# Kernel tuning notes

Hardware: AMD Instinct MI355X
Metric: run time of the kernel (lower is better)

Reference implementation:

```python
import jax, jax.numpy as jnp
import numpy as np
from math import sqrt

D_MODEL = 1024
NUM_HEADS = 16
MASK_VAL = -100000000.0


def setup_inputs() -> dict:
    key = jax.random.key(0)
    k1, k2, k3, k4, k5 = jax.random.split(key, 5)
    scale = 1.0 / sqrt(D_MODEL)
    return {
        "in_features": jax.random.normal(k1, (2, 2048, D_MODEL), dtype=jnp.float32),
        "q_proj_weight": jax.random.normal(k2, (D_MODEL, D_MODEL), dtype=jnp.float32) * scale,
        "k_proj_weight": jax.random.normal(k3, (D_MODEL, D_MODEL), dtype=jnp.float32) * scale,
        "v_proj_weight": jax.random.normal(k4, (D_MODEL, D_MODEL), dtype=jnp.float32) * scale,
        "o_proj_weight": jax.random.normal(k5, (D_MODEL, D_MODEL), dtype=jnp.float32) * scale,
    }


def _proj_heads(x, w, h):
    # x: [b, s, d_in], w: [h*d, d_in] -> [b, h, s, d]
    d = w.shape[0] // h
    w = w.reshape(h, d, w.shape[1])
    return jnp.einsum('bsi,hdi->bhsd', x, w)


def reference(in_features, q_proj_weight, k_proj_weight, v_proj_weight, o_proj_weight):
    h = NUM_HEADS
    b, s, _ = in_features.shape
    q = _proj_heads(in_features, q_proj_weight, h)  # [b,h,s,dk]
    k = _proj_heads(in_features, k_proj_weight, h)
    v = _proj_heads(in_features, v_proj_weight, h)
    d_k = q.shape[-1]
    # additive causal mask: -1e8 above diagonal
    mask = jnp.triu(jnp.full((s, s), MASK_VAL, dtype=q.dtype), k=1)[None, None]
    scores = jnp.einsum('bhqd,bhkd->bhqk', q, k) / sqrt(d_k) + mask
    attn = jax.nn.softmax(scores, axis=-1)
    out = jnp.einsum('bhqk,bhkd->bhqd', attn, v)          # [b,h,s,dv]
    out = out.transpose(0, 2, 1, 3).reshape(b, s, -1)      # [b,s,h*dv]
    return jnp.einsum('bsv,mv->bsm', out, o_proj_weight)
```

## Files before the change

kernel.cpp:

```cpp
#include <hip/hip_runtime.h>
#include <hip/hip_bf16.h>
#include <stdint.h>
#include <type_traits>

typedef __bf16 bf16;
typedef __bf16 bf16x4 __attribute__((ext_vector_type(4)));
typedef __bf16 bf16x8 __attribute__((ext_vector_type(8)));
typedef float floatx4 __attribute__((ext_vector_type(4)));
typedef unsigned int u32;

#define D_MODEL 1024
#define SEQ 2048
#define NHEADS 16
#define DH 64
#define BATCH 2
#define MROWS (BATCH * SEQ)

#define XELEMS ((size_t)MROWS * D_MODEL)
#define WELEMS ((size_t)D_MODEL * D_MODEL)
#define CVT_ELEMS (XELEMS + 4 * WELEMS)

__device__ __forceinline__ void gload_lds16(const void* g, void* l) {
  __builtin_amdgcn_global_load_lds(
      (const __attribute__((address_space(1))) u32*)g,
      (__attribute__((address_space(3))) u32*)l, 16, 0, 0);
}

__global__ __launch_bounds__(256) void cvt_f32_bf16(
    const float* __restrict__ s0, const float* __restrict__ s1,
    const float* __restrict__ s2, const float* __restrict__ s3,
    const float* __restrict__ s4, bf16* __restrict__ dst) {
  const size_t i = ((size_t)blockIdx.x * 256 + threadIdx.x) * 8;
  const float* src;
  size_t off;
  if (i < XELEMS) {
    src = s0; off = i;
  } else {
    const size_t j = i - XELEMS;
    const int r = (int)(j / WELEMS);
    src = (r == 0) ? s1 : (r == 1) ? s2 : (r == 2) ? s3 : s4;
    off = j - (size_t)r * WELEMS;
  }
  floatx4 f0 = *(const floatx4*)&src[off];
  floatx4 f1 = *(const floatx4*)&src[off + 4];
  bf16x8 o;
#pragma unroll
  for (int j = 0; j < 4; j++) { o[j] = (bf16)f0[j]; o[4 + j] = (bf16)f1[j]; }
  *(bf16x8*)&dst[i] = o;
}

#define QKV_ASLOT (256 * 64)
#define QKV_SLOT  (256 * 64 + 128 * 64)

__global__ __launch_bounds__(512) void gemm_qkv(
    const bf16* __restrict__ A, const bf16* __restrict__ W,
    bf16* __restrict__ Qo, bf16* __restrict__ Ko, bf16* __restrict__ Vto) {
  __shared__ bf16 sm[3 * QKV_SLOT];

  const int tid = threadIdx.x;
  const int lane = tid & 63;
  const int w = tid >> 6;
  const int lo16 = lane & 15;
  const int quad = lane >> 4;
  const int wy = w >> 1;
  const int wx = w & 1;

  const int n0 = blockIdx.x * 128;
  const int m0 = blockIdx.y * 256;

  const int sl = lane >> 3;
  const int sc = ((lane & 7) ^ sl) * 8;

  const floatx4 fz = {0.f, 0.f, 0.f, 0.f};
  floatx4 acc[4][4];
#pragma unroll
  for (int i = 0; i < 4; i++)
#pragma unroll
    for (int j = 0; j < 4; j++) acc[i][j] = fz;

  auto stage = [&](int t, int s) {
    bf16* As = &sm[s * QKV_SLOT];
    bf16* Bs = As + QKV_ASLOT;
    const int k0 = t * 64;
#pragma unroll
    for (int i = 0; i < 4; i++) {
      const int seg = w * 4 + i;
      const int row = seg * 8 + sl;
      gload_lds16(&A[(size_t)(m0 + row) * 1024 + k0 + sc], &As[seg * 512]);
    }
#pragma unroll
    for (int i = 0; i < 2; i++) {
      const int seg = w * 2 + i;
      const int row = seg * 8 + sl;
      gload_lds16(&W[(size_t)(n0 + row) * 1024 + k0 + sc], &Bs[seg * 512]);
    }
  };

  auto compute = [&](int s, auto vt) {
    constexpr bool VT = decltype(vt)::value;
    const bf16* As = &sm[s * QKV_SLOT];
    const bf16* Bs = As + QKV_ASLOT;
#pragma unroll
    for (int kk = 0; kk < 64; kk += 32) {
      bf16x8 af[4], bfr[4];
      const int cc = (kk >> 3) + quad;
#pragma unroll
      for (int t = 0; t < 4; t++) {
        const int ra = wy * 64 + t * 16 + lo16;
        const int rb = wx * 64 + t * 16 + lo16;
        af[t]  = *(const bf16x8*)&As[ra * 64 + ((cc ^ (ra & 7)) << 3)];
        bfr[t] = *(const bf16x8*)&Bs[rb * 64 + ((cc ^ (rb & 7)) << 3)];
      }
#pragma unroll
      for (int mt = 0; mt < 4; mt++)
#pragma unroll
        for (int nt = 0; nt < 4; nt++) {
          if constexpr (VT)
            acc[mt][nt] = __builtin_amdgcn_mfma_f32_16x16x32_bf16(bfr[nt], af[mt], acc[mt][nt], 0, 0, 0);
          else
            acc[mt][nt] = __builtin_amdgcn_mfma_f32_16x16x32_bf16(af[mt], bfr[nt], acc[mt][nt], 0, 0, 0);
        }
    }
  };

  auto step = [&](int t, int s, auto vt) {
    if (t + 2 < 16) stage(t + 2, (t + 2) % 3);
    compute(s, vt);
    if (t < 15) {
      if (t + 2 < 16) { asm volatile("s_waitcnt vmcnt(6)" ::: "memory"); }
      else            { asm volatile("s_waitcnt vmcnt(0)" ::: "memory"); }
      __builtin_amdgcn_s_barrier();
    }
  };

  auto mainloop = [&](auto vt) {
    stage(0, 0);
    stage(1, 1);
    asm volatile("s_waitcnt vmcnt(6)" ::: "memory");
    __builtin_amdgcn_s_barrier();
    for (int tb = 0; tb < 15; tb += 3) {
      step(tb + 0, 0, vt);
      step(tb + 1, 1, vt);
      step(tb + 2, 2, vt);
    }
    step(15, 0, vt);
  };
  if (n0 >= 2048) mainloop(std::true_type{}); else mainloop(std::false_type{});

  if (n0 < 2048) {
    bf16* C = (n0 < 1024) ? Qo : Ko;
    const int nc = (n0 < 1024) ? n0 : n0 - 1024;
#pragma unroll
    for (int mt = 0; mt < 4; mt++)
#pragma unroll
      for (int nt = 0; nt < 4; nt++)
#pragma unroll
        for (int r = 0; r < 4; r++) {
          const int row = m0 + wy * 64 + mt * 16 + quad * 4 + r;
          const int col = nc + wx * 64 + nt * 16 + lo16;
          C[(size_t)row * D_MODEL + col] = (bf16)acc[mt][nt][r];
        }
  } else {
    const int nv = n0 - 2048;
#pragma unroll
    for (int mt = 0; mt < 4; mt++)
#pragma unroll
      for (int nt = 0; nt < 4; nt++)
#pragma unroll
        for (int r = 0; r < 4; r++) {
          const int feat = nv + wx * 64 + nt * 16 + quad * 4 + r;
          const int tok  = m0 + wy * 64 + mt * 16 + lo16;
          const int hh = feat >> 6, dd = feat & 63;
          const int bb = tok >> 11, ss = tok & 2047;
          Vto[(size_t)((bb * NHEADS + hh) * DH + dd) * SEQ + ss] = (bf16)acc[mt][nt][r];
        }
  }
}

__global__ __launch_bounds__(256) void gemm_o(
    const bf16* __restrict__ A, const bf16* __restrict__ W,
    float* __restrict__ C) {
  __shared__ bf16 As[2 * 64 * 64];
  __shared__ bf16 Bs[2 * 128 * 64];

  const int tid = threadIdx.x;
  const int lane = tid & 63;
  const int w = tid >> 6;
  const int lo16 = lane & 15;
  const int quad = lane >> 4;
  const int wy = w >> 1, wx = w & 1;

  const int m0 = blockIdx.y * 64;
  const int n0 = blockIdx.x * 128;

  const int sl = lane >> 3;
  const int sc = ((lane & 7) ^ sl) * 8;

  const floatx4 fz = {0.f, 0.f, 0.f, 0.f};
  floatx4 acc[2][4];
#pragma unroll
  for (int i = 0; i < 2; i++)
#pragma unroll
    for (int j = 0; j < 4; j++) acc[i][j] = fz;

  for (int k0 = 0; k0 < 1024; k0 += 128) {
    __syncthreads();
#pragma unroll
    for (int kh = 0; kh < 2; kh++) {
#pragma unroll
      for (int i = 0; i < 2; i++) {
        const int seg = i * 4 + w;
        const int row = seg * 8 + sl;
        gload_lds16(&A[(size_t)(m0 + row) * 1024 + k0 + kh * 64 + sc],
                    &As[kh * 4096 + seg * 512]);
      }
#pragma unroll
      for (int i = 0; i < 4; i++) {
        const int seg = i * 4 + w;
        const int row = seg * 8 + sl;
        gload_lds16(&W[(size_t)(n0 + row) * 1024 + k0 + kh * 64 + sc],
                    &Bs[kh * 8192 + seg * 512]);
      }
    }
    __syncthreads();

#pragma unroll
    for (int kk = 0; kk < 128; kk += 32) {
      const int kh = kk >> 6;
      const int cc = ((kk & 63) >> 3) + quad;
      bf16x8 af[2], bfr[4];
#pragma unroll
      for (int t = 0; t < 2; t++) {
        const int ra = wy * 32 + t * 16 + lo16;
        af[t] = *(const bf16x8*)&As[kh * 4096 + ra * 64 + ((cc ^ (ra & 7)) << 3)];
      }
#pragma unroll
      for (int t = 0; t < 4; t++) {
        const int rb = wx * 64 + t * 16 + lo16;
        bfr[t] = *(const bf16x8*)&Bs[kh * 8192 + rb * 64 + ((cc ^ (rb & 7)) << 3)];
      }
#pragma unroll
      for (int mt = 0; mt < 2; mt++)
#pragma unroll
        for (int nt = 0; nt < 4; nt++)
          acc[mt][nt] = __builtin_amdgcn_mfma_f32_16x16x32_bf16(af[mt], bfr[nt], acc[mt][nt], 0, 0, 0);
    }
  }

#pragma unroll
  for (int mt = 0; mt < 2; mt++)
#pragma unroll
    for (int nt = 0; nt < 4; nt++)
#pragma unroll
      for (int r = 0; r < 4; r++) {
        const int row = m0 + wy * 32 + mt * 16 + quad * 4 + r;
        const int col = n0 + wx * 64 + nt * 16 + lo16;
        C[(size_t)row * D_MODEL + col] = acc[mt][nt][r];
      }
}

#define LPK 72
#define LPV 136
#define LPP 72

__global__ __launch_bounds__(512, 4) void attn_causal(
    const bf16* __restrict__ Q, const bf16* __restrict__ Kg,
    const bf16* __restrict__ Vt, bf16* __restrict__ O) {
  __shared__ __align__(16) char smem[54272];
  bf16* Ks  = (bf16*)smem;
  bf16* VTs = (bf16*)(smem + 18432);
  bf16* Ps  = (bf16*)(smem + 35840);
  float* Es = (float*)smem;

  const int tid = threadIdx.x;
  const int lane = tid & 63;
  const int wid = tid >> 6;
  const int g = wid >> 2;
  const int w4 = wid & 3;
  const int lo16 = lane & 15;
  const int quad = lane >> 4;

  const int x = blockIdx.x;
  const int qtA = x;
  const int qtB = 31 - x;
  const int nA = (qtA + 2) >> 1;
  const int nB = (qtB + 2) >> 1;
  const int h = blockIdx.y;
  const int b = blockIdx.z;
  const size_t base  = (size_t)b * SEQ * D_MODEL + (size_t)h * DH;
  const size_t baset = (size_t)(b * NHEADS + h) * DH * SEQ;

  const int rA = qtA * 64 + w4 * 16 + lo16;
  const int rB = qtB * 64 + w4 * 16 + lo16;
  bf16x8 qfA[2], qfB[2];
#pragma unroll
  for (int ks = 0; ks < 2; ks++) {
    qfA[ks] = *(const bf16x8*)&Q[base + (size_t)rA * D_MODEL + ks * 32 + quad * 8];
    qfB[ks] = *(const bf16x8*)&Q[base + (size_t)rB * D_MODEL + ks * 32 + quad * 8];
  }

  bf16x8 onesf;
#pragma unroll
  for (int j = 0; j < 8; j++) onesf[j] = (bf16)1.0f;

  const floatx4 fz = {0.f, 0.f, 0.f, 0.f};
  floatx4 oA[4], oB[4];
  floatx4 lA = fz, lB = fz;
#pragma unroll
  for (int i = 0; i < 4; i++) { oA[i] = fz; oB[i] = fz; }

  const int kr = tid >> 3;
  const int kc = (tid & 7) * 8;

  bf16x8 kvp[2], vvp[2];
#pragma unroll
  for (int c2 = 0; c2 < 2; c2++) {
    kvp[c2] = *(const bf16x8*)&Kg[base + (size_t)(c2 * 64 + kr) * D_MODEL + kc];
    vvp[c2] = *(const bf16x8*)&Vt[baset + (size_t)kr * SEQ + c2 * 64 + kc];
  }

  for (int c = 0; c < nB; c++) {
    const int j0 = c * 128;
    __syncthreads();
#pragma unroll
    for (int c2 = 0; c2 < 2; c2++) {
      *(bf16x8*)&Ks[(c2 * 64 + kr) * LPK + kc] = kvp[c2];
      *(bf16x8*)&VTs[kr * LPV + c2 * 64 + kc] = vvp[c2];
    }
    __syncthreads();

    if (c + 1 < nB) {
      const int j1 = j0 + 128;
#pragma unroll
      for (int c2 = 0; c2 < 2; c2++) {
        kvp[c2] = *(const bf16x8*)&Kg[base + (size_t)(j1 + c2 * 64 + kr) * D_MODEL + kc];
        vvp[c2] = *(const bf16x8*)&Vt[baset + (size_t)kr * SEQ + j1 + c2 * 64 + kc];
      }
    }

    auto compute = [&](int q0s, const bf16x8* qf, floatx4* oacc, floatx4& lacc,
                       bool diag) {
      floatx4 sacc[4];
#pragma unroll
      for (int n = 0; n < 4; n++) sacc[n] = fz;
#pragma unroll
      for (int n = 0; n < 4; n++) {
        const int rk = g * 64 + n * 16 + lo16;
#pragma unroll
        for (int ks = 0; ks < 2; ks++) {
          bf16x8 kf = *(const bf16x8*)&Ks[rk * LPK + ks * 32 + quad * 8];
          sacc[n] = __builtin_amdgcn_mfma_f32_16x16x32_bf16(kf, qf[ks], sacc[n], 0, 0, 0);
        }
      }

      if (diag) {
        const int myq = q0s + w4 * 16 + lo16;
#pragma unroll
        for (int n = 0; n < 4; n++) {
          const int kvb = j0 + g * 64 + n * 16 + quad * 4;
          bf16x4 pk;
#pragma unroll
          for (int r = 0; r < 4; r++) {
            const float e = __builtin_amdgcn_exp2f(fmaf(sacc[n][r], 0.18033688f, -17.3123405f));
            pk[r] = (bf16)((kvb + r > myq) ? 0.f : e);
          }
          *(bf16x4*)&Ps[wid * 1152 + lo16 * LPP + n * 16 + quad * 4] = pk;
        }
      } else {
#pragma unroll
        for (int n = 0; n < 4; n++) {
          bf16x4 pk;
#pragma unroll
          for (int r = 0; r < 4; r++)
            pk[r] = (bf16)__builtin_amdgcn_exp2f(fmaf(sacc[n][r], 0.18033688f, -17.3123405f));
          *(bf16x4*)&Ps[wid * 1152 + lo16 * LPP + n * 16 + quad * 4] = pk;
        }
      }

#pragma unroll
      for (int ks = 0; ks < 2; ks++) {
        bf16x8 pf = *(const bf16x8*)&Ps[wid * 1152 + lo16 * LPP + ks * 32 + quad * 8];
#pragma unroll
        for (int dt = 0; dt < 4; dt++) {
          bf16x8 vf = *(const bf16x8*)&VTs[(dt * 16 + lo16) * LPV + g * 64 + ks * 32 + quad * 8];
          oacc[dt] = __builtin_amdgcn_mfma_f32_16x16x32_bf16(pf, vf, oacc[dt], 0, 0, 0);
        }
        lacc = __builtin_amdgcn_mfma_f32_16x16x32_bf16(pf, onesf, lacc, 0, 0, 0);
      }
    };

    compute(qtB * 64, qfB, oB, lB, c == nB - 1);
    if (c < nA) compute(qtA * 64, qfA, oA, lA, c == nA - 1);
  }

  __syncthreads();
  if (g == 1) {
    float* e = &Es[(w4 * 64 + lane) * 40];
#pragma unroll
    for (int dt = 0; dt < 4; dt++)
#pragma unroll
      for (int r = 0; r < 4; r++) e[dt * 4 + r] = oA[dt][r];
#pragma unroll
    for (int r = 0; r < 4; r++) e[16 + r] = lA[r];
#pragma unroll
    for (int dt = 0; dt < 4; dt++)
#pragma unroll
      for (int r = 0; r < 4; r++) e[20 + dt * 4 + r] = oB[dt][r];
#pragma unroll
    for (int r = 0; r < 4; r++) e[36 + r] = lB[r];
  }
  __syncthreads();
  if (g == 0) {
    const float* e = &Es[(w4 * 64 + lane) * 40];
#pragma unroll
    for (int dt = 0; dt < 4; dt++)
#pragma unroll
      for (int r = 0; r < 4; r++) { oA[dt][r] += e[dt * 4 + r]; oB[dt][r] += e[20 + dt * 4 + r]; }
#pragma unroll
    for (int r = 0; r < 4; r++) { lA[r] += e[16 + r]; lB[r] += e[36 + r]; }

    auto finish = [&](int q0s, floatx4* oacc, floatx4 lacc) {
#pragma unroll
      for (int r = 0; r < 4; r++) {
        const float inv = 1.0f / lacc[r];
        const int row = q0s + w4 * 16 + quad * 4 + r;
#pragma unroll
        for (int dt = 0; dt < 4; dt++)
          O[base + (size_t)row * D_MODEL + dt * 16 + lo16] = (bf16)(oacc[dt][r] * inv);
      }
    };
    finish(qtA * 64, oA, lA);
    finish(qtB * 64, oB, lB);
  }
}

extern "C" void kernel_launch(void* const* d_in, const int* in_sizes, int n_in,
                              void* d_out, int out_size, void* d_ws, size_t ws_size,
                              hipStream_t stream) {
  const float* X  = (const float*)d_in[0];
  const float* Wq = (const float*)d_in[1];
  const float* Wk = (const float*)d_in[2];
  const float* Wv = (const float*)d_in[3];
  const float* Wo = (const float*)d_in[4];
  float* out = (float*)d_out;

  bf16* cvt = (bf16*)d_ws;
  bf16* Xb  = cvt;
  bf16* Wqb = cvt + XELEMS;
  bf16* Wob = Wqb + 3 * WELEMS;
  bf16* Qb  = cvt + CVT_ELEMS;
  bf16* Kb  = Qb + XELEMS;
  bf16* Vtb = Kb + XELEMS;
  bf16* Ob  = Vtb + XELEMS;

  dim3 blk(256);
  cvt_f32_bf16<<<dim3((u32)(CVT_ELEMS / (256 * 8))), blk, 0, stream>>>(
      X, Wq, Wk, Wv, Wo, cvt);
  gemm_qkv<<<dim3(24, 16), dim3(512), 0, stream>>>(Xb, Wqb, Qb, Kb, Vtb);
  attn_causal<<<dim3(16, NHEADS, BATCH), dim3(512), 0, stream>>>(Qb, Kb, Vtb, Ob);
  gemm_o<<<dim3(8, 64), blk, 0, stream>>>(Ob, Wob, out);
}
```

Measured before the change: 168.5 us.

## Keep P in registers via permlane swaps; one query tile per block

The attention kernel no longer stages the exp'd score tile P through shared memory. It packs pairs of values with v_cvt_pk_bf16_f32 and rearranges them into the MFMA A-operand layout with v_permlane32/16_swap, removing an LDS write/read round trip per chunk. The paired-tile load balancing (tile x with tile 31-x) is dropped: the grid doubles to 32 blocks per head, each handling one query tile, and launch bounds rise to 6 blocks per SM with less shared memory. This exposes more parallelism and occupancy, but each K/V chunk is loaded once per query tile instead of once per pair, and per-block work becomes unbalanced.

```diff
diff --git a/kernel.cpp b/kernel.cpp
--- a/kernel.cpp
+++ b/kernel.cpp
@@ -8,6 +8,7 @@
 typedef __bf16 bf16x8 __attribute__((ext_vector_type(8)));
 typedef float floatx4 __attribute__((ext_vector_type(4)));
 typedef unsigned int u32;
+typedef u32 u32x4 __attribute__((ext_vector_type(4)));
 
 #define D_MODEL 1024
 #define SEQ 2048
@@ -261,15 +262,13 @@
 
 #define LPK 72
 #define LPV 136
-#define LPP 72
-
-__global__ __launch_bounds__(512, 4) void attn_causal(
+
+__global__ __launch_bounds__(512, 6) void attn_causal(
     const bf16* __restrict__ Q, const bf16* __restrict__ Kg,
     const bf16* __restrict__ Vt, bf16* __restrict__ O) {
-  __shared__ __align__(16) char smem[54272];
+  __shared__ __align__(16) char smem[35840];
   bf16* Ks  = (bf16*)smem;
   bf16* VTs = (bf16*)(smem + 18432);
-  bf16* Ps  = (bf16*)(smem + 35840);
   float* Es = (float*)smem;
 
   const int tid = threadIdx.x;
@@ -280,34 +279,28 @@
   const int lo16 = lane & 15;
   const int quad = lane >> 4;
 
-  const int x = blockIdx.x;
-  const int qtA = x;
-  const int qtB = 31 - x;
-  const int nA = (qtA + 2) >> 1;
-  const int nB = (qtB + 2) >> 1;
+  const int qt = 31 - blockIdx.x;
+  const int n = (qt + 2) >> 1;
   const int h = blockIdx.y;
   const int b = blockIdx.z;
   const size_t base  = (size_t)b * SEQ * D_MODEL + (size_t)h * DH;
   const size_t baset = (size_t)(b * NHEADS + h) * DH * SEQ;
 
-  const int rA = qtA * 64 + w4 * 16 + lo16;
-  const int rB = qtB * 64 + w4 * 16 + lo16;
-  bf16x8 qfA[2], qfB[2];
-#pragma unroll
-  for (int ks = 0; ks < 2; ks++) {
-    qfA[ks] = *(const bf16x8*)&Q[base + (size_t)rA * D_MODEL + ks * 32 + quad * 8];
-    qfB[ks] = *(const bf16x8*)&Q[base + (size_t)rB * D_MODEL + ks * 32 + quad * 8];
-  }
+  const int rq = qt * 64 + w4 * 16 + lo16;
+  bf16x8 qf[2];
+#pragma unroll
+  for (int ks = 0; ks < 2; ks++)
+    qf[ks] = *(const bf16x8*)&Q[base + (size_t)rq * D_MODEL + ks * 32 + quad * 8];
 
   bf16x8 onesf;
 #pragma unroll
   for (int j = 0; j < 8; j++) onesf[j] = (bf16)1.0f;
 
   const floatx4 fz = {0.f, 0.f, 0.f, 0.f};
-  floatx4 oA[4], oB[4];
-  floatx4 lA = fz, lB = fz;
-#pragma unroll
-  for (int i = 0; i < 4; i++) { oA[i] = fz; oB[i] = fz; }
+  floatx4 oacc[4];
+  floatx4 lacc = fz;
+#pragma unroll
+  for (int i = 0; i < 4; i++) oacc[i] = fz;
 
   const int kr = tid >> 3;
   const int kc = (tid & 7) * 8;
@@ -319,7 +312,7 @@
     vvp[c2] = *(const bf16x8*)&Vt[baset + (size_t)kr * SEQ + c2 * 64 + kc];
   }
 
-  for (int c = 0; c < nB; c++) {
+  for (int c = 0; c < n; c++) {
     const int j0 = c * 128;
     __syncthreads();
 #pragma unroll
@@ -329,7 +322,7 @@
     }
     __syncthreads();
 
-    if (c + 1 < nB) {
+    if (c + 1 < n) {
       const int j1 = j0 + 128;
 #pragma unroll
       for (int c2 = 0; c2 < 2; c2++) {
@@ -338,99 +331,93 @@
       }
     }
 
-    auto compute = [&](int q0s, const bf16x8* qf, floatx4* oacc, floatx4& lacc,
-                       bool diag) {
-      floatx4 sacc[4];
-#pragma unroll
-      for (int n = 0; n < 4; n++) sacc[n] = fz;
-#pragma unroll
-      for (int n = 0; n < 4; n++) {
-        const int rk = g * 64 + n * 16 + lo16;
-#pragma unroll
-        for (int ks = 0; ks < 2; ks++) {
-          bf16x8 kf = *(const bf16x8*)&Ks[rk * LPK + ks * 32 + quad * 8];
-          sacc[n] = __builtin_amdgcn_mfma_f32_16x16x32_bf16(kf, qf[ks], sacc[n], 0, 0, 0);
+    floatx4 sacc[4];
+#pragma unroll
+    for (int n4 = 0; n4 < 4; n4++) sacc[n4] = fz;
+#pragma unroll
+    for (int n4 = 0; n4 < 4; n4++) {
+      const int rk = g * 64 + n4 * 16 + lo16;
+#pragma unroll
+      for (int ks = 0; ks < 2; ks++) {
+        bf16x8 kf = *(const bf16x8*)&Ks[rk * LPK + ks * 32 + quad * 8];
+        sacc[n4] = __builtin_amdgcn_mfma_f32_16x16x32_bf16(kf, qf[ks], sacc[n4], 0, 0, 0);
+      }
+    }
+
+    u32 wv[4][2];
+    if (c == n - 1) {
+      const int myq = rq;
+#pragma unroll
+      for (int n4 = 0; n4 < 4; n4++) {
+        float e[4];
+#pragma unroll
+        for (int r = 0; r < 4; r++) {
+          const int kvb = j0 + g * 64 + n4 * 16 + quad * 4 + r;
+          const float ev = __builtin_amdgcn_exp2f(fmaf(sacc[n4][r], 0.18033688f, -17.3123405f));
+          e[r] = (kvb > myq) ? 0.f : ev;
         }
-      }
-
-      if (diag) {
-        const int myq = q0s + w4 * 16 + lo16;
-#pragma unroll
-        for (int n = 0; n < 4; n++) {
-          const int kvb = j0 + g * 64 + n * 16 + quad * 4;
-          bf16x4 pk;
-#pragma unroll
-          for (int r = 0; r < 4; r++) {
-            const float e = __builtin_amdgcn_exp2f(fmaf(sacc[n][r], 0.18033688f, -17.3123405f));
-            pk[r] = (bf16)((kvb + r > myq) ? 0.f : e);
-          }
-          *(bf16x4*)&Ps[wid * 1152 + lo16 * LPP + n * 16 + quad * 4] = pk;
-        }
-      } else {
-#pragma unroll
-        for (int n = 0; n < 4; n++) {
-          bf16x4 pk;
-#pragma unroll
-          for (int r = 0; r < 4; r++)
-            pk[r] = (bf16)__builtin_amdgcn_exp2f(fmaf(sacc[n][r], 0.18033688f, -17.3123405f));
-          *(bf16x4*)&Ps[wid * 1152 + lo16 * LPP + n * 16 + quad * 4] = pk;
-        }
-      }
-
-#pragma unroll
-      for (int ks = 0; ks < 2; ks++) {
-        bf16x8 pf = *(const bf16x8*)&Ps[wid * 1152 + lo16 * LPP + ks * 32 + quad * 8];
-#pragma unroll
-        for (int dt = 0; dt < 4; dt++) {
-          bf16x8 vf = *(const bf16x8*)&VTs[(dt * 16 + lo16) * LPV + g * 64 + ks * 32 + quad * 8];
-          oacc[dt] = __builtin_amdgcn_mfma_f32_16x16x32_bf16(pf, vf, oacc[dt], 0, 0, 0);
-        }
-        lacc = __builtin_amdgcn_mfma_f32_16x16x32_bf16(pf, onesf, lacc, 0, 0, 0);
-      }
-    };
-
-    compute(qtB * 64, qfB, oB, lB, c == nB - 1);
-    if (c < nA) compute(qtA * 64, qfA, oA, lA, c == nA - 1);
+        asm("v_cvt_pk_bf16_f32 %0, %1, %2" : "=v"(wv[n4][0]) : "v"(e[0]), "v"(e[1]));
+        asm("v_cvt_pk_bf16_f32 %0, %1, %2" : "=v"(wv[n4][1]) : "v"(e[2]), "v"(e[3]));
+      }
+    } else {
+#pragma unroll
+      for (int n4 = 0; n4 < 4; n4++) {
+        float e[4];
+#pragma unroll
+        for (int r = 0; r < 4; r++)
+          e[r] = __builtin_amdgcn_exp2f(fmaf(sacc[n4][r], 0.18033688f, -17.3123405f));
+        asm("v_cvt_pk_bf16_f32 %0, %1, %2" : "=v"(wv[n4][0]) : "v"(e[0]), "v"(e[1]));
+        asm("v_cvt_pk_bf16_f32 %0, %1, %2" : "=v"(wv[n4][1]) : "v"(e[2]), "v"(e[3]));
+      }
+    }
+
+#pragma unroll
+    for (int ks = 0; ks < 2; ks++) {
+      u32 a0 = wv[2 * ks][0], b0 = wv[2 * ks + 1][0];
+      u32 a1 = wv[2 * ks][1], b1 = wv[2 * ks + 1][1];
+      asm("v_permlane32_swap_b32 %0, %1" : "+v"(a0), "+v"(b0));
+      asm("v_permlane16_swap_b32 %0, %1" : "+v"(a0), "+v"(b0));
+      asm("v_permlane32_swap_b32 %0, %1" : "+v"(a1), "+v"(b1));
+      asm("v_permlane16_swap_b32 %0, %1" : "+v"(a1), "+v"(b1));
+      u32x4 fw = {a0, a1, b0, b1};
+      const bf16x8 pf = __builtin_bit_cast(bf16x8, fw);
+#pragma unroll
+      for (int dt = 0; dt < 4; dt++) {
+        bf16x8 vf = *(const bf16x8*)&VTs[(dt * 16 + lo16) * LPV + g * 64 + ks * 32 + quad * 8];
+        oacc[dt] = __builtin_amdgcn_mfma_f32_16x16x32_bf16(pf, vf, oacc[dt], 0, 0, 0);
+      }
+      lacc = __builtin_amdgcn_mfma_f32_16x16x32_bf16(pf, onesf, lacc, 0, 0, 0);
+    }
   }
 
   __syncthreads();
   if (g == 1) {
-    float* e = &Es[(w4 * 64 + lane) * 40];
+    float* e = &Es[(w4 * 64 + lane) * 21];
 #pragma unroll
     for (int dt = 0; dt < 4; dt++)
 #pragma unroll
-      for (int r = 0; r < 4; r++) e[dt * 4 + r] = oA[dt][r];
-#pragma unroll
-    for (int r = 0; r < 4; r++) e[16 + r] = lA[r];
-#pragma unroll
-    for (int dt = 0; dt < 4; dt++)
-#pragma unroll
-      for (int r = 0; r < 4; r++) e[20 + dt * 4 + r] = oB[dt][r];
-#pragma unroll
-    for (int r = 0; r < 4; r++) e[36 + r] = lB[r];
+      for (int r = 0; r < 4; r++) e[dt * 4 + r] = oacc[dt][r];
+#pragma unroll
+    for (int r = 0; r < 4; r++) e[16 + r] = lacc[r];
   }
   __syncthreads();
   if (g == 0) {
-    const float* e = &Es[(w4 * 64 + lane) * 40];
+    const float* e = &Es[(w4 * 64 + lane) * 21];
 #pragma unroll
     for (int dt = 0; dt < 4; dt++)
 #pragma unroll
-      for (int r = 0; r < 4; r++) { oA[dt][r] += e[dt * 4 + r]; oB[dt][r] += e[20 + dt * 4 + r]; }
-#pragma unroll
-    for (int r = 0; r < 4; r++) { lA[r] += e[16 + r]; lB[r] += e[36 + r]; }
-
-    auto finish = [&](int q0s, floatx4* oacc, floatx4 lacc) {
-#pragma unroll
-      for (int r = 0; r < 4; r++) {
-        const float inv = 1.0f / lacc[r];
-        const int row = q0s + w4 * 16 + quad * 4 + r;
-#pragma unroll
-        for (int dt = 0; dt < 4; dt++)
-          O[base + (size_t)row * D_MODEL + dt * 16 + lo16] = (bf16)(oacc[dt][r] * inv);
-      }
-    };
-    finish(qtA * 64, oA, lA);
-    finish(qtB * 64, oB, lB);
+      for (int r = 0; r < 4; r++) oacc[dt][r] += e[dt * 4 + r];
+#pragma unroll
+    for (int r = 0; r < 4; r++) lacc[r] += e[16 + r];
+
+#pragma unroll
+    for (int r = 0; r < 4; r++) {
+      const float inv = 1.0f / lacc[r];
+      const int row = qt * 64 + w4 * 16 + quad * 4 + r;
+#pragma unroll
+      for (int dt = 0; dt < 4; dt++)
+        O[base + (size_t)row * D_MODEL + dt * 16 + lo16] = (bf16)(oacc[dt][r] * inv);
+    }
   }
 }
 
@@ -457,6 +444,6 @@
   cvt_f32_bf16<<<dim3((u32)(CVT_ELEMS / (256 * 8))), blk, 0, stream>>>(
       X, Wq, Wk, Wv, Wo, cvt);
   gemm_qkv<<<dim3(24, 16), dim3(512), 0, stream>>>(Xb, Wqb, Qb, Kb, Vtb);
-  attn_causal<<<dim3(16, NHEADS, BATCH), dim3(512), 0, stream>>>(Qb, Kb, Vtb, Ob);
+  attn_causal<<<dim3(32, NHEADS, BATCH), dim3(512), 0, stream>>>(Qb, Kb, Vtb, Ob);
   gemm_o<<<dim3(8, 64), blk, 0, stream>>>(Ob, Wob, out);
 }
```

After: 193.8 us. 1.15x slower.

## Keep softmax probabilities in registers via permlane swaps instead of LDS round-trip

Applied to the files above, without the earlier changes.

Replaces the per-wave LDS staging of the bf16 probability tile with an in-register relayout. Packed bf16 conversions are followed by v_permlane32/16_swap, so the P fragment becomes the A operand of the PV MFMA directly. This removes LDS writes and reads and shrinks shared memory by the P buffer. It also drops the occupancy hint from launch_bounds and pads the epilogue exchange stride to 41 to avoid bank conflicts. The cost is added register pressure and reliance on the exact lane permutation semantics for correctness.

```diff
diff --git a/kernel.cpp b/kernel.cpp
--- a/kernel.cpp
+++ b/kernel.cpp
@@ -8,6 +8,7 @@
 typedef __bf16 bf16x8 __attribute__((ext_vector_type(8)));
 typedef float floatx4 __attribute__((ext_vector_type(4)));
 typedef unsigned int u32;
+typedef u32 u32x4 __attribute__((ext_vector_type(4)));
 
 #define D_MODEL 1024
 #define SEQ 2048
@@ -261,15 +262,13 @@
 
 #define LPK 72
 #define LPV 136
-#define LPP 72
-
-__global__ __launch_bounds__(512, 4) void attn_causal(
+
+__global__ __launch_bounds__(512) void attn_causal(
     const bf16* __restrict__ Q, const bf16* __restrict__ Kg,
     const bf16* __restrict__ Vt, bf16* __restrict__ O) {
-  __shared__ __align__(16) char smem[54272];
+  __shared__ __align__(16) char smem[41984];
   bf16* Ks  = (bf16*)smem;
   bf16* VTs = (bf16*)(smem + 18432);
-  bf16* Ps  = (bf16*)(smem + 35840);
   float* Es = (float*)smem;
 
   const int tid = threadIdx.x;
@@ -342,44 +341,54 @@
                        bool diag) {
       floatx4 sacc[4];
 #pragma unroll
-      for (int n = 0; n < 4; n++) sacc[n] = fz;
-#pragma unroll
-      for (int n = 0; n < 4; n++) {
-        const int rk = g * 64 + n * 16 + lo16;
+      for (int n4 = 0; n4 < 4; n4++) sacc[n4] = fz;
+#pragma unroll
+      for (int n4 = 0; n4 < 4; n4++) {
+        const int rk = g * 64 + n4 * 16 + lo16;
 #pragma unroll
         for (int ks = 0; ks < 2; ks++) {
           bf16x8 kf = *(const bf16x8*)&Ks[rk * LPK + ks * 32 + quad * 8];
-          sacc[n] = __builtin_amdgcn_mfma_f32_16x16x32_bf16(kf, qf[ks], sacc[n], 0, 0, 0);
-        }
-      }
-
+          sacc[n4] = __builtin_amdgcn_mfma_f32_16x16x32_bf16(kf, qf[ks], sacc[n4], 0, 0, 0);
+        }
+      }
+
+      u32 wv[4][2];
       if (diag) {
         const int myq = q0s + w4 * 16 + lo16;
 #pragma unroll
-        for (int n = 0; n < 4; n++) {
-          const int kvb = j0 + g * 64 + n * 16 + quad * 4;
-          bf16x4 pk;
+        for (int n4 = 0; n4 < 4; n4++) {
+          float e[4];
 #pragma unroll
           for (int r = 0; r < 4; r++) {
-            const float e = __builtin_amdgcn_exp2f(fmaf(sacc[n][r], 0.18033688f, -17.3123405f));
-            pk[r] = (bf16)((kvb + r > myq) ? 0.f : e);
+            const int kvb = j0 + g * 64 + n4 * 16 + quad * 4 + r;
+            const float ev = __builtin_amdgcn_exp2f(fmaf(sacc[n4][r], 0.18033688f, -17.3123405f));
+            e[r] = (kvb > myq) ? 0.f : ev;
           }
-          *(bf16x4*)&Ps[wid * 1152 + lo16 * LPP + n * 16 + quad * 4] = pk;
+          asm("v_cvt_pk_bf16_f32 %0, %1, %2" : "=v"(wv[n4][0]) : "v"(e[0]), "v"(e[1]));
+          asm("v_cvt_pk_bf16_f32 %0, %1, %2" : "=v"(wv[n4][1]) : "v"(e[2]), "v"(e[3]));
         }
       } else {
 #pragma unroll
-        for (int n = 0; n < 4; n++) {
-          bf16x4 pk;
+        for (int n4 = 0; n4 < 4; n4++) {
+          float e[4];
 #pragma unroll
           for (int r = 0; r < 4; r++)
-            pk[r] = (bf16)__builtin_amdgcn_exp2f(fmaf(sacc[n][r], 0.18033688f, -17.3123405f));
-          *(bf16x4*)&Ps[wid * 1152 + lo16 * LPP + n * 16 + quad * 4] = pk;
+            e[r] = __builtin_amdgcn_exp2f(fmaf(sacc[n4][r], 0.18033688f, -17.3123405f));
+          asm("v_cvt_pk_bf16_f32 %0, %1, %2" : "=v"(wv[n4][0]) : "v"(e[0]), "v"(e[1]));
+          asm("v_cvt_pk_bf16_f32 %0, %1, %2" : "=v"(wv[n4][1]) : "v"(e[2]), "v"(e[3]));
         }
       }
 
 #pragma unroll
       for (int ks = 0; ks < 2; ks++) {
-        bf16x8 pf = *(const bf16x8*)&Ps[wid * 1152 + lo16 * LPP + ks * 32 + quad * 8];
+        u32 a0 = wv[2 * ks][0], b0 = wv[2 * ks + 1][0];
+        u32 a1 = wv[2 * ks][1], b1 = wv[2 * ks + 1][1];
+        asm("v_permlane32_swap_b32 %0, %1" : "+v"(a0), "+v"(b0));
+        asm("v_permlane16_swap_b32 %0, %1" : "+v"(a0), "+v"(b0));
+        asm("v_permlane32_swap_b32 %0, %1" : "+v"(a1), "+v"(b1));
+        asm("v_permlane16_swap_b32 %0, %1" : "+v"(a1), "+v"(b1));
+        u32x4 fw = {a0, a1, b0, b1};
+        const bf16x8 pf = __builtin_bit_cast(bf16x8, fw);
 #pragma unroll
         for (int dt = 0; dt < 4; dt++) {
           bf16x8 vf = *(const bf16x8*)&VTs[(dt * 16 + lo16) * LPV + g * 64 + ks * 32 + quad * 8];
@@ -395,7 +404,7 @@
 
   __syncthreads();
   if (g == 1) {
-    float* e = &Es[(w4 * 64 + lane) * 40];
+    float* e = &Es[(w4 * 64 + lane) * 41];
 #pragma unroll
     for (int dt = 0; dt < 4; dt++)
 #pragma unroll
@@ -411,7 +420,7 @@
   }
   __syncthreads();
   if (g == 0) {
-    const float* e = &Es[(w4 * 64 + lane) * 40];
+    const float* e = &Es[(w4 * 64 + lane) * 41];
 #pragma unroll
     for (int dt = 0; dt < 4; dt++)
 #pragma unroll
```

Measured after the change: 170.2 us (median of 2 runs). Within noise of the previous version (+1.0%).
